# Kernel optimization log

Measured on AMD Instinct MI355X. Metric: run time of the kernel, lower is better.

## Reference

```python
import jax, jax.numpy as jnp
import numpy as np

L = 512      # number of residues
Q = 21       # alphabet size (20 AAs + gap)
N = 4096     # number of sequences
RES = 400    # residue_idx: number of already-known sites (< L)
BETA = 1.0   # inverse temperature


def setup_inputs() -> dict:
    key = jax.random.key(0)
    k_tok, k_h, k_J = jax.random.split(key, 3)
    # One-hot encoded partial MSA: [N, RES, Q]
    tokens = jax.random.randint(k_tok, (N, RES), 0, Q)
    X = jax.nn.one_hot(tokens, Q, dtype=jnp.float32)
    # Learned parameters (init scale 1e-4 as in the torch module)
    h = jax.random.normal(k_h, (L, Q), dtype=jnp.float32) * 1e-4
    J = jax.random.normal(k_J, (L, Q, L, Q), dtype=jnp.float32) * 1e-4
    return {"X": X, "h": h, "J": J}


def reference(X, h, J):
    # residue_idx = X.shape[1] (static under jit)
    n_samples, i, q = X.shape
    # J[i, :, :i, :] -> [q, i*q]; X -> [n, i*q]
    J_ar = J[i, :, :i, :].reshape(q, i * q)
    logit_i = h[i] + jnp.einsum('ij,nj->ni', J_ar, X.reshape(n_samples, i * q))
    return jax.nn.softmax(BETA * logit_i, axis=-1)  # [n, q]
```

## Files before the change

kernel.cpp:

```cpp
#include <hip/hip_runtime.h>


#define QA    21
#define RESI  400
#define NSEQ  4096
#define NT    12
#define NBX   342
#define NCH   5
#define CHJ   80
#define SJ    16
#define NST   5
#define STAGE_F  (NT*SJ*QA)
#define STAGE_V4 (STAGE_F/4)
#define JQ2_ELEMS (RESI*QA*QA)
#define P_PER (NT*QA)
#define P_ELEMS (NCH*NBX*P_PER)

#define GLOAD_LDS16(g, l)                                                     \
    __builtin_amdgcn_global_load_lds(                                         \
        (const __attribute__((address_space(1))) void*)(g),                   \
        (__attribute__((address_space(3))) void*)(l), 16, 0, 0)

__global__ __launch_bounds__(256) void k0_jq2(const float* __restrict__ J,
                                              float* __restrict__ Jq2) {
    int s = blockIdx.x * 256 + threadIdx.x;
    if (s >= JQ2_ELEMS) return;
    int q  = s / 8400;
    int ja = s - q * 8400;
    Jq2[ja * 21 + q] = J[(8400 + q) * 10752 + ja];
}

__global__ __launch_bounds__(256) void k1_main(const float* __restrict__ X,
                                               const float* __restrict__ Jq2,
                                               float* __restrict__ P) {
    __shared__ float buf[2][STAGE_F];
    __shared__ int   tokb[2][NT * SJ];

    const int tid = threadIdx.x;
    const int bx  = blockIdx.x;
    const int c   = blockIdx.y;
    const int n0  = bx * NT;
    const int j0  = c * CHJ;

    const int w    = tid >> 6, l = tid & 63;
    const int q    = l % 21;
    const int ns   = l / 21;
    const int nloc = w * 3 + ns;
    const bool act = (l < 63);

    auto issue = [&](int s) {
        const int jb = j0 + s * SJ;
        float* dst = &buf[s & 1][0];
        #pragma unroll
        for (int k = 0; k < 4; ++k) {
            int e = tid + (k << 8);
            if (e < STAGE_V4) {
                int row = e / 84;
                int col = e - row * 84;
                int nr  = n0 + row;
                if (nr >= NSEQ) nr = n0;
                const float* gp = X + (nr * RESI + jb) * QA + (col << 2);
                GLOAD_LDS16(gp, dst + (e << 2));
            }
        }
    };

    float acc = 0.f;
    issue(0);

    #pragma unroll
    for (int s = 0; s < NST; ++s) {
        const int p = s & 1;
        if (s + 1 < NST) {
            issue(s + 1);
            asm volatile("s_waitcnt vmcnt(4)" ::: "memory");
        } else {
            asm volatile("s_waitcnt vmcnt(0)" ::: "memory");
        }
        __builtin_amdgcn_s_barrier();
        __builtin_amdgcn_sched_barrier(0);

        if (tid < NT * SJ) {
            const int r = tid >> 4, jj = tid & 15;
            const float* cell = &buf[p][r * (SJ * QA) + jj * QA];
            float fa = 0.f;
            #pragma unroll
            for (int a = 0; a < QA; ++a) fa = fmaf(cell[a], (float)a, fa);
            tokb[p][tid] = (int)(fa + 0.5f);
        }
        asm volatile("s_waitcnt lgkmcnt(0)" ::: "memory");
        __builtin_amdgcn_s_barrier();
        __builtin_amdgcn_sched_barrier(0);

        if (act) {
            const int jb441 = (j0 + s * SJ) * 441;
            const int4* tp = (const int4*)&tokb[p][nloc * SJ];
            #pragma unroll
            for (int g = 0; g < 4; ++g) {
                int4 t4 = tp[g];
                acc += Jq2[jb441 + (4 * g + 0) * 441 + t4.x * 21 + q];
                acc += Jq2[jb441 + (4 * g + 1) * 441 + t4.y * 21 + q];
                acc += Jq2[jb441 + (4 * g + 2) * 441 + t4.z * 21 + q];
                acc += Jq2[jb441 + (4 * g + 3) * 441 + t4.w * 21 + q];
            }
        }
    }

    float* pb = &buf[0][0];
    if (act) pb[q * NT + nloc] = acc;
    __syncthreads();
    if (tid < P_PER)
        P[(c * NBX + bx) * P_PER + tid] = pb[tid];
}

__global__ __launch_bounds__(256) void k2_finish(const float* __restrict__ P,
                                                 const float* __restrict__ h,
                                                 float* __restrict__ out) {
    __shared__ float sm[P_PER];
    const int bx = blockIdx.x, tid = threadIdx.x;
    if (tid < P_PER) {
        float v = 0.f;
        #pragma unroll
        for (int cc = 0; cc < NCH; ++cc)
            v += P[(cc * NBX + bx) * P_PER + tid];
        sm[tid] = v + h[8400 + tid / NT];
    }
    __syncthreads();
    if (tid < P_PER) {
        const int nl = tid / QA, q2 = tid - nl * QA;
        const int n  = bx * NT + nl;
        if (n < NSEQ) {
            float m = -1e30f;
            #pragma unroll
            for (int a = 0; a < QA; ++a) m = fmaxf(m, sm[a * NT + nl]);
            float den = 0.f;
            #pragma unroll
            for (int a = 0; a < QA; ++a) den += __expf(sm[a * NT + nl] - m);
            out[n * QA + q2] = __expf(sm[q2 * NT + nl] - m) / den;
        }
    }
}

extern "C" void kernel_launch(void* const* d_in, const int* in_sizes, int n_in,
                              void* d_out, int out_size, void* d_ws, size_t ws_size,
                              hipStream_t stream) {
    const float* X = (const float*)d_in[0];
    const float* h = (const float*)d_in[1];
    const float* J = (const float*)d_in[2];
    float* out = (float*)d_out;

    float* Jq2 = (float*)d_ws;
    float* P   = Jq2 + JQ2_ELEMS;

    k0_jq2<<<(JQ2_ELEMS + 255) / 256, 256, 0, stream>>>(J, Jq2);
    k1_main<<<dim3(NBX, NCH), 256, 0, stream>>>(X, Jq2, P);
    k2_finish<<<NBX, 256, 0, stream>>>(P, h, out);
}
```

Before: 40.02 us.

## Fuse softmax into main kernel and drop j-chunk split reduction

Each block now covers 6 sequences and all 400 known residues in 25 stages, instead of 12 sequences over one of 5 j-chunks. The per-chunk partial buffer and the separate finish kernel are removed. Bias add and softmax run at the end of the main kernel. This saves one launch and the partial-sum round trip through global memory, but each block now runs a longer serial loop (no longer unrolled) with fewer total blocks (683 vs 1710) and smaller 128-thread blocks, so latency hiding may suffer.

```diff
diff --git a/kernel.cpp b/kernel.cpp
--- a/kernel.cpp
+++ b/kernel.cpp
@@ -4,17 +4,13 @@
 #define QA    21
 #define RESI  400
 #define NSEQ  4096
-#define NT    12
-#define NBX   342
-#define NCH   5
-#define CHJ   80
+#define NT    6
+#define NBX   683
 #define SJ    16
-#define NST   5
+#define NST   25
 #define STAGE_F  (NT*SJ*QA)
 #define STAGE_V4 (STAGE_F/4)
 #define JQ2_ELEMS (RESI*QA*QA)
-#define P_PER (NT*QA)
-#define P_ELEMS (NCH*NBX*P_PER)
 
 #define GLOAD_LDS16(g, l)                                                     \
     __builtin_amdgcn_global_load_lds(                                         \
@@ -30,17 +26,16 @@
     Jq2[ja * 21 + q] = J[(8400 + q) * 10752 + ja];
 }
 
-__global__ __launch_bounds__(256) void k1_main(const float* __restrict__ X,
+__global__ __launch_bounds__(128) void k1_main(const float* __restrict__ X,
                                                const float* __restrict__ Jq2,
-                                               float* __restrict__ P) {
+                                               const float* __restrict__ h,
+                                               float* __restrict__ out) {
     __shared__ float buf[2][STAGE_F];
     __shared__ int   tokb[2][NT * SJ];
+    __shared__ float lg[NT * QA];
 
     const int tid = threadIdx.x;
-    const int bx  = blockIdx.x;
-    const int c   = blockIdx.y;
-    const int n0  = bx * NT;
-    const int j0  = c * CHJ;
+    const int n0  = blockIdx.x * NT;
 
     const int w    = tid >> 6, l = tid & 63;
     const int q    = l % 21;
@@ -49,11 +44,11 @@
     const bool act = (l < 63);
 
     auto issue = [&](int s) {
-        const int jb = j0 + s * SJ;
+        const int jb = s * SJ;
         float* dst = &buf[s & 1][0];
         #pragma unroll
         for (int k = 0; k < 4; ++k) {
-            int e = tid + (k << 8);
+            int e = tid + (k << 7);
             if (e < STAGE_V4) {
                 int row = e / 84;
                 int col = e - row * 84;
@@ -68,7 +63,6 @@
     float acc = 0.f;
     issue(0);
 
-    #pragma unroll
     for (int s = 0; s < NST; ++s) {
         const int p = s & 1;
         if (s + 1 < NST) {
@@ -93,7 +87,7 @@
         __builtin_amdgcn_sched_barrier(0);
 
         if (act) {
-            const int jb441 = (j0 + s * SJ) * 441;
+            const int jb441 = s * (SJ * 441);
             const int4* tp = (const int4*)&tokb[p][nloc * SJ];
             #pragma unroll
             for (int g = 0; g < 4; ++g) {
@@ -106,37 +100,20 @@
         }
     }
 
-    float* pb = &buf[0][0];
-    if (act) pb[q * NT + nloc] = acc;
+    if (act) lg[nloc * QA + q] = acc + h[8400 + q];
     __syncthreads();
-    if (tid < P_PER)
-        P[(c * NBX + bx) * P_PER + tid] = pb[tid];
-}
-
-__global__ __launch_bounds__(256) void k2_finish(const float* __restrict__ P,
-                                                 const float* __restrict__ h,
-                                                 float* __restrict__ out) {
-    __shared__ float sm[P_PER];
-    const int bx = blockIdx.x, tid = threadIdx.x;
-    if (tid < P_PER) {
-        float v = 0.f;
-        #pragma unroll
-        for (int cc = 0; cc < NCH; ++cc)
-            v += P[(cc * NBX + bx) * P_PER + tid];
-        sm[tid] = v + h[8400 + tid / NT];
-    }
-    __syncthreads();
-    if (tid < P_PER) {
+    if (tid < NT * QA) {
         const int nl = tid / QA, q2 = tid - nl * QA;
-        const int n  = bx * NT + nl;
+        const int n  = n0 + nl;
         if (n < NSEQ) {
+            const float* rowp = lg + nl * QA;
             float m = -1e30f;
             #pragma unroll
-            for (int a = 0; a < QA; ++a) m = fmaxf(m, sm[a * NT + nl]);
+            for (int a = 0; a < QA; ++a) m = fmaxf(m, rowp[a]);
             float den = 0.f;
             #pragma unroll
-            for (int a = 0; a < QA; ++a) den += __expf(sm[a * NT + nl] - m);
-            out[n * QA + q2] = __expf(sm[q2 * NT + nl] - m) / den;
+            for (int a = 0; a < QA; ++a) den += __expf(rowp[a] - m);
+            out[n * QA + q2] = __expf(rowp[q2] - m) / den;
         }
     }
 }
@@ -150,9 +127,7 @@
     float* out = (float*)d_out;
 
     float* Jq2 = (float*)d_ws;
-    float* P   = Jq2 + JQ2_ELEMS;
 
     k0_jq2<<<(JQ2_ELEMS + 255) / 256, 256, 0, stream>>>(J, Jq2);
-    k1_main<<<dim3(NBX, NCH), 256, 0, stream>>>(X, Jq2, P);
-    k2_finish<<<NBX, 256, 0, stream>>>(P, h, out);
+    k1_main<<<NBX, 128, 0, stream>>>(X, Jq2, h, out);
 }
```

Result: slower. 44.35 us (+10.8%).
